# Optimization experiments

Hardware: AMD Instinct MI355X
Metric: run time of the kernel (lower is better)

## Reference

```python
import jax, jax.numpy as jnp
import numpy as np

ALPHA = 0.5
SPECTRAL_RADIUS = 0.9
INPUT_SIZE = 64
RESERVOIR_SIZE = 1024
OUTPUT_SIZE = 64
BATCH = 512
SEQ_LEN = 512


def setup_inputs() -> dict:
    key = jax.random.key(0)
    k_in, k_res, k_win, k_wout = jax.random.split(key, 4)
    inp = jax.random.normal(k_in, (BATCH, SEQ_LEN, INPUT_SIZE), dtype=jnp.float32)
    # uniform(-1, 1) init, then rescale W_reservoir to target spectral radius
    W_res = jax.random.uniform(k_res, (RESERVOIR_SIZE, RESERVOIR_SIZE), minval=-1.0, maxval=1.0, dtype=jnp.float32)
    radius = np.max(np.abs(np.linalg.eigvals(np.asarray(W_res, dtype=np.float64))))
    W_res = W_res * jnp.float32(SPECTRAL_RADIUS / radius)
    W_in = jax.random.uniform(k_win, (INPUT_SIZE, RESERVOIR_SIZE), minval=-1.0, maxval=1.0, dtype=jnp.float32)
    W_out = jax.random.uniform(k_wout, (RESERVOIR_SIZE, OUTPUT_SIZE), minval=-1.0, maxval=1.0, dtype=jnp.float32)
    return {"input": inp, "W_reservoir": W_res, "W_in": W_in, "W_out": W_out}


def reference(input, W_reservoir, W_in, W_out):
    alpha = jnp.float32(ALPHA)
    batch = input.shape[0]
    res = W_reservoir.shape[0]
    # precompute input projections for all timesteps: [B,T,I] @ [I,R] -> [B,T,R]
    u_proj = jnp.einsum("bti,ir->btr", input, W_in)
    u_seq = jnp.transpose(u_proj, (1, 0, 2))  # [T,B,R]

    def step(state, u_t):
        new_state = (1.0 - alpha) * state + alpha * jnp.tanh(state @ W_reservoir + u_t)
        return new_state, None

    init = jnp.zeros((batch, res), dtype=input.dtype)
    final_state, _ = jax.lax.scan(step, init, u_seq)
    return final_state @ W_out
```

## Files before the change

### kernel.cpp

```cpp
#include <hip/hip_runtime.h>

#define B_   512
#define T_   512
#define I_   64
#define R_   1024
#define O_   64
#define KK_  34
#define NT_STRIDE 17408

typedef __attribute__((ext_vector_type(8))) short short8;
typedef __attribute__((ext_vector_type(4))) float float4v;

__device__ inline unsigned short f2bf(float x) {
  union { float f; unsigned u; } v; v.f = x;
  unsigned r = v.u + 0x7FFFu + ((v.u >> 16) & 1u);
  return (unsigned short)(r >> 16);
}
__device__ inline float bf2f(unsigned short h) {
  union { unsigned u; float f; } v; v.u = ((unsigned)h) << 16;
  return v.f;
}
__device__ inline float ftanh(float x) {
  float e = __expf(2.0f * x);
  return 1.0f - 2.0f / (e + 1.0f);
}

__device__ inline size_t wt2_idx(int k, int n) {
  return ((((size_t)(n >> 4) * KK_ + (k >> 5)) * 4 + ((k >> 3) & 3)) * 16 + (n & 15)) * 8 + (k & 7);
}

__global__ void esn_prep_wt(const float* __restrict__ Wres, const float* __restrict__ Win,
                            unsigned short* __restrict__ Wt2) {
  __shared__ float tile[32][33];
  int nt = blockIdx.x, kt = blockIdx.y;
  int tx = threadIdx.x & 31;
  int ty = threadIdx.x >> 5;
  int k0 = kt * 32, n0 = nt * 32;
  #pragma unroll
  for (int s = 0; s < 4; ++s) {
    int k = k0 + ty + 8 * s;
    int n = n0 + tx;
    float v = (k < R_) ? Wres[(size_t)k * R_ + n] : Win[(size_t)(k - R_) * R_ + n];
    tile[ty + 8 * s][tx] = v;
  }
  __syncthreads();
  #pragma unroll
  for (int s = 0; s < 4; ++s) {
    int n = n0 + ty + 8 * s;
    int k = k0 + tx;
    Wt2[wt2_idx(k, n)] = f2bf(tile[tx][ty + 8 * s]);
  }
}

__global__ __launch_bounds__(1024, 4) void esn_recur(
    const float* __restrict__ input, const unsigned short* __restrict__ Wt2,
    const float* __restrict__ Wout, float* __restrict__ out) {
  __shared__ unsigned short aLds[KK_ * 4 * 16 * 8];

  int tid  = threadIdx.x;
  int lane = tid & 63;
  int w    = tid >> 6;
  int nl   = lane & 15;
  int kgrp = lane >> 4;
  int bg0  = blockIdx.x * 16;

  int m_u = tid >> 6;
  int i_u = tid & 63;
  int k_u = R_ + i_u;
  int idx_u = (((k_u >> 5) * 4 + ((k_u >> 3) & 3)) * 16 + m_u) * 8 + (k_u & 7);
  const float* inp_u = input + ((size_t)(bg0 + m_u) * T_) * I_ + i_u;

  int* zp = (int*)aLds;
  #pragma unroll
  for (int s = 0; s < 8; ++s) zp[tid + 1024 * s] = 0;
  aLds[idx_u] = f2bf(inp_u[0]);
  __syncthreads();

  const unsigned short* aBase = aLds + ((size_t)kgrp * 16 + nl) * 8;
  const unsigned short* bBase = Wt2 + (size_t)(w * 4) * NT_STRIDE + kgrp * 128 + nl * 8;

  float s_local[4][4];
  #pragma unroll
  for (int nn = 0; nn < 4; ++nn)
    #pragma unroll
    for (int r = 0; r < 4; ++r) s_local[nn][r] = 0.f;

  for (int t = 0; t < T_; ++t) {
    float un = (t < T_ - 1) ? inp_u[(size_t)(t + 1) * I_] : 0.f;

    float4v acc[4];
    #pragma unroll
    for (int nn = 0; nn < 4; ++nn) acc[nn] = (float4v){0.f, 0.f, 0.f, 0.f};

    #pragma unroll 2
    for (int kk = 0; kk < KK_; ++kk) {
      short8 a = *(const short8*)(aBase + kk * 512);
      #pragma unroll
      for (int nn = 0; nn < 4; ++nn) {
        short8 b = *(const short8*)(bBase + (size_t)nn * NT_STRIDE + kk * 512);
        acc[nn] = __builtin_amdgcn_mfma_f32_16x16x32_bf16(a, b, acc[nn], 0, 0, 0);
      }
    }

    __syncthreads();

    #pragma unroll
    for (int nn = 0; nn < 4; ++nn) {
      int n_g = w * 64 + nn * 16 + nl;
      int base = (((n_g >> 5) * 4 + ((n_g >> 3) & 3)) * 16) * 8 + (n_g & 7);
      #pragma unroll
      for (int r = 0; r < 4; ++r) {
        int m = kgrp * 4 + r;
        float ns = 0.5f * s_local[nn][r] + 0.5f * ftanh(acc[nn][r]);
        s_local[nn][r] = ns;
        aLds[base + m * 8] = f2bf(ns);
      }
    }
    aLds[idx_u] = f2bf(un);
    __syncthreads();
  }

  int o = tid & 63, mo = tid >> 6;
  const float* wo = Wout + o;
  float accO = 0.f;
  #pragma unroll 8
  for (int r = 0; r < R_; ++r) {
    int idx = (((r >> 5) * 4 + ((r >> 3) & 3)) * 16 + mo) * 8 + (r & 7);
    accO += bf2f(aLds[idx]) * wo[(size_t)r * O_];
  }
  out[(size_t)(bg0 + mo) * O_ + o] = accO;
}

extern "C" void kernel_launch(void* const* d_in, const int* in_sizes, int n_in,
                              void* d_out, int out_size, void* d_ws, size_t ws_size,
                              hipStream_t stream) {
  const float* input = (const float*)d_in[0];
  const float* Wres  = (const float*)d_in[1];
  const float* Win   = (const float*)d_in[2];
  const float* Wout  = (const float*)d_in[3];
  float* out = (float*)d_out;

  unsigned short* Wt2 = (unsigned short*)d_ws;

  esn_prep_wt<<<dim3(32, 34), 256, 0, stream>>>(Wres, Win, Wt2);
  esn_recur<<<32, 1024, 0, stream>>>(input, Wt2, Wout, out);
}
```

Before: 9.109 ms.

## Split reservoir columns across cooperative blocks with register-resident weights and global barriers

The recurrence is spread over 256 cooperative blocks instead of 32. Eight blocks share each 16-row batch group, and each block owns 128 output columns whose bf16 weight fragments stay in registers across all timesteps. Each step's new state is written to a double-buffered global buffer and synchronised through per-timestep atomic counters with polling, then copied back into LDS. This removes the repeated weight streaming from L2 each step. In exchange it adds a cross-block barrier and a global round trip every timestep, plus a bounded spin that could yield wrong results if blocks are not co-resident.

```diff
diff --git a/kernel.cpp b/kernel.cpp
--- a/kernel.cpp
+++ b/kernel.cpp
@@ -1,12 +1,12 @@
 #include <hip/hip_runtime.h>
 
-#define B_   512
 #define T_   512
 #define I_   64
 #define R_   1024
 #define O_   64
 #define KK_  34
-#define NT_STRIDE 17408
+#define GRP_ 8
+#define POLL_MAX 65536
 
 typedef __attribute__((ext_vector_type(8))) short short8;
 typedef __attribute__((ext_vector_type(4))) float float4v;
@@ -52,83 +52,129 @@
   }
 }
 
-__global__ __launch_bounds__(1024, 4) void esn_recur(
+__global__ void esn_zero_cnt(int* __restrict__ cnt) {
+  cnt[blockIdx.x * 1024 + threadIdx.x] = 0;
+}
+
+__global__ __launch_bounds__(512, 2) void esn_recur_x(
     const float* __restrict__ input, const unsigned short* __restrict__ Wt2,
-    const float* __restrict__ Wout, float* __restrict__ out) {
-  __shared__ unsigned short aLds[KK_ * 4 * 16 * 8];
-
-  int tid  = threadIdx.x;
-  int lane = tid & 63;
-  int w    = tid >> 6;
-  int nl   = lane & 15;
-  int kgrp = lane >> 4;
-  int bg0  = blockIdx.x * 16;
-
-  int m_u = tid >> 6;
-  int i_u = tid & 63;
-  int k_u = R_ + i_u;
-  int idx_u = (((k_u >> 5) * 4 + ((k_u >> 3) & 3)) * 16 + m_u) * 8 + (k_u & 7);
-  const float* inp_u = input + ((size_t)(bg0 + m_u) * T_) * I_ + i_u;
+    const float* __restrict__ Wout, float* __restrict__ out,
+    unsigned short* __restrict__ sbuf, int* __restrict__ cnt) {
+  __shared__ unsigned short aLds[KK_ * 512];
+
+  const int tid  = threadIdx.x;
+  const int lane = tid & 63;
+  const int w    = tid >> 6;
+  const int nl   = lane & 15;
+  const int kgrp = lane >> 4;
+  const int bid  = blockIdx.x;
+  const int gb   = bid & 31;
+  const int gc   = bid >> 5;
+  const int bg0  = gb * 16;
+
+  const int nt = gc * 8 + w;
+  const unsigned short* bBase = Wt2 + (size_t)nt * 17408 + kgrp * 128 + nl * 8;
+  short8 wfrag[KK_];
+  #pragma unroll
+  for (int kk = 0; kk < KK_; ++kk) wfrag[kk] = *(const short8*)(bBase + kk * 512);
+
+  const int m_u = tid >> 5;
+  const int i0  = (tid & 31) * 2;
+  const float* inp_u = input + (size_t)(bg0 + m_u) * T_ * I_ + i0;
+  const int k_u = R_ + i0;
+  const int idxu = (((k_u >> 5) * 4 + ((k_u >> 3) & 3)) * 16 + m_u) * 8 + (k_u & 7);
 
   int* zp = (int*)aLds;
   #pragma unroll
-  for (int s = 0; s < 8; ++s) zp[tid + 1024 * s] = 0;
-  aLds[idx_u] = f2bf(inp_u[0]);
+  for (int s = 0; s < 16; ++s) zp[tid + 512 * s] = 0;
+  {
+    float2 u0 = *(const float2*)inp_u;
+    *(unsigned*)(aLds + idxu) = (unsigned)f2bf(u0.x) | ((unsigned)f2bf(u0.y) << 16);
+  }
   __syncthreads();
 
-  const unsigned short* aBase = aLds + ((size_t)kgrp * 16 + nl) * 8;
-  const unsigned short* bBase = Wt2 + (size_t)(w * 4) * NT_STRIDE + kgrp * 128 + nl * 8;
-
-  float s_local[4][4];
-  #pragma unroll
-  for (int nn = 0; nn < 4; ++nn)
+  const unsigned short* aBase = aLds + (kgrp * 16 + nl) * 8;
+  const int n_g = gc * 128 + w * 16 + nl;
+  const int pub = (((n_g >> 5) * 4 + ((n_g >> 3) & 3)) * 16 + kgrp * 4) * 8 + (n_g & 7);
+  int* const cbase = cnt + gb * T_;
+  unsigned short* const sb0 = sbuf + (size_t)gb * 16384;
+  unsigned short* const sb1 = sbuf + 524288 + (size_t)gb * 16384;
+
+  float s_local[4] = {0.f, 0.f, 0.f, 0.f};
+
+  for (int t = 0; t < T_; ++t) {
+    const int tn = (t + 1 < T_) ? t + 1 : T_ - 1;
+    float2 un = *(const float2*)(inp_u + (size_t)tn * I_);
+
+    float4v acc = {0.f, 0.f, 0.f, 0.f};
     #pragma unroll
-    for (int r = 0; r < 4; ++r) s_local[nn][r] = 0.f;
-
-  for (int t = 0; t < T_; ++t) {
-    float un = (t < T_ - 1) ? inp_u[(size_t)(t + 1) * I_] : 0.f;
-
-    float4v acc[4];
-    #pragma unroll
-    for (int nn = 0; nn < 4; ++nn) acc[nn] = (float4v){0.f, 0.f, 0.f, 0.f};
-
-    #pragma unroll 2
     for (int kk = 0; kk < KK_; ++kk) {
       short8 a = *(const short8*)(aBase + kk * 512);
+      acc = __builtin_amdgcn_mfma_f32_16x16x32_bf16(a, wfrag[kk], acc, 0, 0, 0);
+    }
+
+    unsigned short* dst = ((t & 1) ? sb0 : sb1) + pub;
+    #pragma unroll
+    for (int r = 0; r < 4; ++r) {
+      float ns = 0.5f * s_local[r] + 0.5f * ftanh(acc[r]);
+      s_local[r] = ns;
+      dst[r * 8] = f2bf(ns);
+    }
+    __syncthreads();
+    if (tid == 0)
+      __hip_atomic_fetch_add(cbase + t, 1, __ATOMIC_RELEASE, __HIP_MEMORY_SCOPE_AGENT);
+
+    if (t + 1 < T_) {
+      if (tid == 0) {
+        int guard = 0;
+        while (__hip_atomic_load(cbase + t, __ATOMIC_RELAXED, __HIP_MEMORY_SCOPE_AGENT) < GRP_
+               && guard < POLL_MAX) {
+          __builtin_amdgcn_s_sleep(1);
+          ++guard;
+        }
+      }
+      __syncthreads();
+      __threadfence();
+      const unsigned short* src = (t & 1) ? sb0 : sb1;
       #pragma unroll
-      for (int nn = 0; nn < 4; ++nn) {
-        short8 b = *(const short8*)(bBase + (size_t)nn * NT_STRIDE + kk * 512);
-        acc[nn] = __builtin_amdgcn_mfma_f32_16x16x32_bf16(a, b, acc[nn], 0, 0, 0);
+      for (int c = 0; c < 4; ++c) {
+        short8 v = *(const short8*)(src + (c * 512 + tid) * 8);
+        *(short8*)(aLds + (c * 512 + tid) * 8) = v;
       }
-    }
-
+      *(unsigned*)(aLds + idxu) = (unsigned)f2bf(un.x) | ((unsigned)f2bf(un.y) << 16);
+      __syncthreads();
+    }
+  }
+
+  if (gc == 0) {
+    if (tid == 0) {
+      int guard = 0;
+      while (__hip_atomic_load(cbase + (T_ - 1), __ATOMIC_RELAXED, __HIP_MEMORY_SCOPE_AGENT) < GRP_
+             && guard < POLL_MAX) {
+        __builtin_amdgcn_s_sleep(1);
+        ++guard;
+      }
+    }
     __syncthreads();
-
+    __threadfence();
     #pragma unroll
-    for (int nn = 0; nn < 4; ++nn) {
-      int n_g = w * 64 + nn * 16 + nl;
-      int base = (((n_g >> 5) * 4 + ((n_g >> 3) & 3)) * 16) * 8 + (n_g & 7);
-      #pragma unroll
-      for (int r = 0; r < 4; ++r) {
-        int m = kgrp * 4 + r;
-        float ns = 0.5f * s_local[nn][r] + 0.5f * ftanh(acc[nn][r]);
-        s_local[nn][r] = ns;
-        aLds[base + m * 8] = f2bf(ns);
-      }
-    }
-    aLds[idx_u] = f2bf(un);
+    for (int c = 0; c < 4; ++c) {
+      short8 v = *(const short8*)(sb0 + (c * 512 + tid) * 8);
+      *(short8*)(aLds + (c * 512 + tid) * 8) = v;
+    }
     __syncthreads();
-  }
-
-  int o = tid & 63, mo = tid >> 6;
-  const float* wo = Wout + o;
-  float accO = 0.f;
-  #pragma unroll 8
-  for (int r = 0; r < R_; ++r) {
-    int idx = (((r >> 5) * 4 + ((r >> 3) & 3)) * 16 + mo) * 8 + (r & 7);
-    accO += bf2f(aLds[idx]) * wo[(size_t)r * O_];
-  }
-  out[(size_t)(bg0 + mo) * O_ + o] = accO;
+    const int m = tid >> 5;
+    const int o0 = (tid & 31) * 2;
+    float a0 = 0.f, a1 = 0.f;
+    for (int k = 0; k < R_; ++k) {
+      float sv = bf2f(aLds[(((k >> 5) * 4 + ((k >> 3) & 3)) * 16 + m) * 8 + (k & 7)]);
+      const float* wr = Wout + (size_t)k * O_ + o0;
+      a0 += sv * wr[0];
+      a1 += sv * wr[1];
+    }
+    float2 res; res.x = a0; res.y = a1;
+    *(float2*)(out + (size_t)(bg0 + m) * O_ + o0) = res;
+  }
 }
 
 extern "C" void kernel_launch(void* const* d_in, const int* in_sizes, int n_in,
@@ -140,8 +186,15 @@
   const float* Wout  = (const float*)d_in[3];
   float* out = (float*)d_out;
 
-  unsigned short* Wt2 = (unsigned short*)d_ws;
+  char* ws = (char*)d_ws;
+  unsigned short* Wt2  = (unsigned short*)ws;
+  unsigned short* sbuf = (unsigned short*)(ws + 2228224);
+  int*            cnt  = (int*)(ws + 2228224 + 2097152);
 
   esn_prep_wt<<<dim3(32, 34), 256, 0, stream>>>(Wres, Win, Wt2);
-  esn_recur<<<32, 1024, 0, stream>>>(input, Wt2, Wout, out);
-}
+  esn_zero_cnt<<<16, 1024, 0, stream>>>(cnt);
+
+  void* args[] = { (void*)&input, (void*)&Wt2, (void*)&Wout, (void*)&out,
+                   (void*)&sbuf, (void*)&cnt };
+  hipLaunchCooperativeKernel((void*)esn_recur_x, dim3(256), dim3(512), args, 0, stream);
+}
```

After: 21.31 ms. 134% more time.
